# Performance work log

Measured on AMD Instinct MI355X. Metric: run time of the kernel, lower is better.

## Reference

```python
import jax, jax.numpy as jnp
from jax import lax
import numpy as np

N, M, S = 16, 32, 128
ALPHA = 1e-06


def _conv(x, w, b, stride):
    y = lax.conv_general_dilated(x, w, (stride, stride), [(1, 1), (1, 1)],
                                 dimension_numbers=('NCHW', 'OIHW', 'NCHW'))
    return y + b[None, :, None, None]


def _deconv(x, w, b):
    # torch ConvTranspose2d(k=4, s=2, p=1); torch weight layout [in, out, kh, kw]
    k = jnp.transpose(w, (1, 0, 2, 3))[:, :, ::-1, ::-1]
    y = lax.conv_general_dilated(x, k, (1, 1), [(2, 2), (2, 2)],
                                 lhs_dilation=(2, 2),
                                 dimension_numbers=('NCHW', 'OIHW', 'NCHW'))
    return y + b[None, :, None, None]


def _kaiming(key, shape):
    fan_in = shape[1] * shape[2] * shape[3]
    return jax.random.normal(key, shape, dtype=jnp.float32) * np.float32(np.sqrt(2.0 / fan_in))


def setup_inputs():
    key = jax.random.key(0)
    ks = jax.random.split(key, 12)
    B, H, W = 8, 256, 256
    return {
        'x': jax.random.normal(ks[0], (B, 3, H, W), dtype=jnp.float32),
        'e0n_w1': _kaiming(ks[1], (N, 3, 3, 3)), 'e0n_b1': jnp.zeros((N,), jnp.float32),
        'e0n_w2': _kaiming(ks[2], (N, N, 3, 3)), 'e0n_b2': jnp.zeros((N,), jnp.float32),
        'e0s_w1': _kaiming(ks[3], (S, 3, 3, 3)), 'e0s_b1': jnp.zeros((S,), jnp.float32),
        'e0s_w2': _kaiming(ks[4], (S, S, 3, 3)), 'e0s_b2': jnp.zeros((S,), jnp.float32),
        'd0_dw': jax.random.normal(ks[5], (S, 3, 4, 4), jnp.float32) * np.float32(np.sqrt(2.0 / (3 * 16))),
        'd0_db': jnp.zeros((3,), jnp.float32),
        'd0_cw': _kaiming(ks[6], (3, 3, 3, 3)), 'd0_cb': jnp.zeros((3,), jnp.float32),
        'cell_k': jax.random.normal(ks[7], (M, N), jnp.float32) / np.float32(np.sqrt(N)),
        'cell_v': jax.random.normal(ks[8], (M, S), jnp.float32) / np.float32(np.sqrt(S)),
    }


def reference(x, e0n_w1, e0n_b1, e0n_w2, e0n_b2, e0s_w1, e0s_b1, e0s_w2, e0s_b2,
              d0_dw, d0_db, d0_cw, d0_cb, cell_k, cell_v):
    silu = jax.nn.silu
    # ConvBlock encoders (stride-2 on second conv)
    e0_n = silu(_conv(silu(_conv(x, e0n_w1, e0n_b1, 1)), e0n_w2, e0n_b2, 2))  # [B,N,H/2,W/2]
    e0_s = silu(_conv(silu(_conv(x, e0s_w1, e0s_b1, 1)), e0s_w2, e0s_b2, 2))  # [B,S,H/2,W/2]
    B, _, H, W = e0_n.shape
    # permute+flatten to token streams (the irregular-access glue)
    z = e0_n.transpose(0, 2, 3, 1).reshape(-1, N)        # [T, N]
    t_star = e0_s.transpose(0, 2, 3, 1).reshape(-1, S)   # [T, S]
    # memcell: softmax key/value retrieval over M slots
    w = jax.nn.softmax(z @ cell_k.T / jnp.sqrt(jnp.float32(N)), axis=-1)  # [T, M]
    t_hat = w @ cell_v                                   # read_update's read (old memory)
    cell_v_new = cell_v + ALPHA * (w.T @ (t_star - t_hat))  # delta-rule value update
    t_read = w @ cell_v_new                              # read(); d1_n == e0_n so weights reused
    d0_m = t_read.reshape(B, H, W, S).transpose(0, 3, 1, 2)  # [B,S,H/2,W/2]
    # DeconvBlock decoder back to 3 channels at full resolution
    d0_n = silu(_conv(silu(_deconv(d0_m, d0_dw, d0_db)), d0_cw, d0_cb, 1))
    return d0_n
```

## Files before the change

### kernel.cpp

```cpp
#include <hip/hip_runtime.h>
#include <hip/hip_bf16.h>


#define ALPHA_F 1e-6f
#define TTOT 131072

typedef __attribute__((ext_vector_type(8))) short bf16x8;
typedef __attribute__((ext_vector_type(4))) float f32x4;

__device__ __forceinline__ float silu_f(float x) {
    return x * __builtin_amdgcn_rcpf(1.f + __expf(-x));
}

__device__ __forceinline__ short f2bf(float f) {
    __hip_bfloat16 h = __float2bfloat16(f);
    union { __hip_bfloat16 b; short s; } u; u.b = h; return u.s;
}

__device__ __forceinline__ float bf2f(unsigned short s) {
    union { unsigned u; float f; } c; c.u = (unsigned)s << 16; return c.f;
}

__device__ __forceinline__ int pack_fp8x4(float a, float b, float c, float d) {
    int lo = __builtin_amdgcn_cvt_pk_fp8_f32(a, b, 0, false);
    return  __builtin_amdgcn_cvt_pk_fp8_f32(c, d, lo, true);
}

template<int CO>
__global__ __launch_bounds__(256) void conv1_silu(
    const float* __restrict__ x, const float* __restrict__ wgt,
    const float* __restrict__ bias, float* __restrict__ out)
{
    int idx = blockIdx.x * 256 + threadIdx.x;
    int w = idx & 255, h = (idx >> 8) & 255, b = idx >> 16;
    const float* xb = x + (size_t)b * 3 * 65536;
    float in[27];
#pragma unroll
    for (int ci = 0; ci < 3; ci++)
#pragma unroll
        for (int ky = 0; ky < 3; ky++)
#pragma unroll
            for (int kx = 0; kx < 3; kx++) {
                int hh = h + ky - 1, ww = w + kx - 1;
                bool ok = ((unsigned)hh < 256u) && ((unsigned)ww < 256u);
                in[(ci * 3 + ky) * 3 + kx] = ok ? xb[(ci << 16) + (hh << 8) + ww] : 0.f;
            }
    float* ob = out + (size_t)b * CO * 65536 + (h << 8) + w;
#pragma unroll 4
    for (int co = 0; co < CO; co++) {
        float acc = bias[co];
#pragma unroll
        for (int k = 0; k < 27; k++) acc += in[k] * wgt[co * 27 + k];
        ob[(size_t)co << 16] = silu_f(acc);
    }
}

#define XPAD_DW 842112
__global__ __launch_bounds__(256) void sprep_kern(
    const float* __restrict__ x, const float* __restrict__ w1,
    unsigned* __restrict__ xpad, unsigned* __restrict__ wbf)
{
    if (blockIdx.x == 3290) {
        int co = threadIdx.x;
        if (co < 128) {
            unsigned short row[28];
#pragma unroll
            for (int k = 0; k < 27; k++) row[k] = (unsigned short)f2bf(w1[co * 27 + k]);
            row[27] = 0;
#pragma unroll
            for (int j = 0; j < 14; j++)
                wbf[co * 20 + j] = (unsigned)row[2 * j] | ((unsigned)row[2 * j + 1] << 16);
#pragma unroll
            for (int j = 14; j < 20; j++) wbf[co * 20 + j] = 0u;
        }
        return;
    }
    int d = blockIdx.x * 256 + threadIdx.x;
    if (d >= XPAD_DW) return;
    int w2 = d % 136;
    int rr = d / 136;
    int hp = rr % 258;
    int plane = rr / 258;
    unsigned val = 0u;
    if (hp >= 1 && hp <= 256 && w2 >= 4 && w2 <= 131) {
        const float* src = x + (size_t)plane * 65536 + (size_t)(hp - 1) * 256 + (2 * w2 - 8);
        float2 f = *(const float2*)src;
        val = (unsigned)(unsigned short)f2bf(f.x) |
              ((unsigned)(unsigned short)f2bf(f.y) << 16);
    }
    xpad[d] = val;
}

#define C1K 40
__global__ __launch_bounds__(256) void conv1s_mfma(
    const unsigned short* __restrict__ xpad, const unsigned short* __restrict__ wbf,
    const float* __restrict__ bias, char* __restrict__ out8)
{
    __shared__ __align__(16) short Ps[128 * C1K];
    int tid = threadIdx.x;
    int g = blockIdx.x;
    int b = g >> 10, rem = g & 1023;
    int hh2 = rem >> 1;
    int h = hh2 >> 1, w0 = (hh2 & 1) * 128;
    int coB = (rem & 1) * 64;

    int lane = tid & 63, wave = tid >> 6;
    int coL = (wave & 1) * 32, pxH = (wave >> 1) * 64;
    int r16 = lane & 15, q = lane >> 4, koff = q * 8;

    bf16x8 af[2];
#pragma unroll
    for (int mt = 0; mt < 2; mt++)
        af[mt] = *(const bf16x8*)&wbf[(coB + coL + mt * 16 + r16) * C1K + koff];

    if (tid < 128) {
        int wpix = w0 + tid;
        const unsigned short* p0 = xpad + ((size_t)(b * 3) * 258 + h) * 272 + 7 + wpix;
        unsigned v[27];
#pragma unroll
        for (int ci = 0; ci < 3; ci++) {
            const unsigned short* pc = p0 + ci * 70176;
#pragma unroll
            for (int ky = 0; ky < 3; ky++)
#pragma unroll
                for (int kx = 0; kx < 3; kx++)
                    v[ci * 9 + ky * 3 + kx] = pc[ky * 272 + kx];
        }
        unsigned dw[16];
#pragma unroll
        for (int i = 0; i < 13; i++) dw[i] = v[2 * i] | (v[2 * i + 1] << 16);
        dw[13] = v[26];
        dw[14] = 0u; dw[15] = 0u;
#pragma unroll
        for (int j = 0; j < 4; j++)
            *(float4*)&Ps[tid * C1K + j * 8] = *(float4*)&dw[j * 4];
    }
    __syncthreads();

    bf16x8 bfr[4];
#pragma unroll
    for (int nt = 0; nt < 4; nt++)
        bfr[nt] = *(bf16x8*)&Ps[(pxH + nt * 16 + r16) * C1K + koff];
    f32x4 acc[2][4];
#pragma unroll
    for (int mt = 0; mt < 2; mt++)
#pragma unroll
        for (int nt = 0; nt < 4; nt++) {
#pragma unroll
            for (int r = 0; r < 4; r++) acc[mt][nt][r] = 0.f;
            acc[mt][nt] = __builtin_amdgcn_mfma_f32_16x16x32_bf16(
                af[mt], bfr[nt], acc[mt][nt], 0, 0, 0);
        }

    int hwb = (h << 8) + w0 + pxH;
    int* ob4 = (int*)out8 + (size_t)b * 8 * 65536 * 4;
#pragma unroll
    for (int mt = 0; mt < 2; mt++) {
        int cb = coB + coL + mt * 16 + q * 4;
        float4 bv = *(const float4*)&bias[cb];
        int cg = (coB + coL + mt * 16) >> 4;
#pragma unroll
        for (int nt = 0; nt < 4; nt++) {
            int hw = hwb + nt * 16 + r16;
            int pk = pack_fp8x4(silu_f(acc[mt][nt][0] + bv.x),
                                silu_f(acc[mt][nt][1] + bv.y),
                                silu_f(acc[mt][nt][2] + bv.z),
                                silu_f(acc[mt][nt][3] + bv.w));
            ob4[((size_t)cg * 65536 + hw) * 4 + q] = pk;
        }
    }
}

__global__ __launch_bounds__(256) void wprep_kern(
    const float* __restrict__ w, int* __restrict__ wt8)
{
    int d = blockIdx.x * 256 + threadIdx.x;
    int pos = d >> 12;
    int rb = (d << 2) & 16383;
    int c16 = rb >> 11, co = (rb >> 4) & 127, e0 = rb & 15;
    float f[4];
#pragma unroll
    for (int j = 0; j < 4; j++) {
        int ci = c16 * 16 + e0 + j;
        f[j] = w[co * 1152 + ci * 9 + pos];
    }
    wt8[d] = pack_fp8x4(f[0], f[1], f[2], f[3]);
}

__global__ __launch_bounds__(256) void conv2s_mfma(
    const char* __restrict__ a8,
    const char* __restrict__ wt8,
    const float* __restrict__ bias, __hip_bfloat16* __restrict__ out)
{
    __shared__ __align__(16) char As[4 * 64 * 16];
    __shared__ __align__(16) char Bs[4 * 128 * 16];
    int tid = threadIdx.x;
    int g = blockIdx.x;
    int b = g >> 8, h2 = (g >> 1) & 127, w2base = (g & 1) * 64;
    int lane = tid & 63, wave = tid >> 6;
    int mrow = lane & 15, q = lane >> 4;

    f32x4 acc[2][4];
#pragma unroll
    for (int i = 0; i < 2; i++)
#pragma unroll
        for (int j = 0; j < 4; j++)
#pragma unroll
            for (int r = 0; r < 4; r++) acc[i][j][r] = 0.f;

    const float4* ab4 = (const float4*)a8 + (size_t)b * 8 * 65536;
    const float4* wb4 = (const float4*)wt8;
    int cA = tid >> 6, tokA = tid & 63;
    int sB0 = tid, sB1 = tid + 256;

#pragma unroll 1
    for (int pos = 0; pos < 9; pos++) {
        int ky = pos / 3, kx = pos - 3 * ky;
        int y = 2 * h2 - 1 + ky;
        if ((unsigned)y >= 256u) continue;
        int x = 2 * (w2base + tokA) - 1 + kx;
        int pix = (y << 8) + (x & 255);
#pragma unroll 1
        for (int cc = 0; cc < 2; cc++) {
            float4 a0 = make_float4(0.f, 0.f, 0.f, 0.f);
            if (x >= 0) a0 = ab4[(size_t)(cc * 4 + cA) * 65536 + pix];
            const float4* brow = wb4 + pos * 1024 + cc * 512;
            float4 b0 = brow[sB0], b1 = brow[sB1];
            __syncthreads();
            *(float4*)&As[tid * 16] = a0;
            *(float4*)&Bs[sB0 * 16] = b0;
            *(float4*)&Bs[sB1 * 16] = b1;
            __syncthreads();
#pragma unroll
            for (int kc = 0; kc < 2; kc++) {
                int cl = kc * 2 + (q >> 1), off = (q & 1) * 8;
                long afr[4], bfr[2];
#pragma unroll
                for (int mt = 0; mt < 4; mt++)
                    afr[mt] = *(long*)&As[(cl * 64 + mt * 16 + mrow) * 16 + off];
#pragma unroll
                for (int nt = 0; nt < 2; nt++)
                    bfr[nt] = *(long*)&Bs[(cl * 128 + wave * 32 + nt * 16 + mrow) * 16 + off];
#pragma unroll
                for (int nt = 0; nt < 2; nt++)
#pragma unroll
                    for (int mt = 0; mt < 4; mt++)
                        acc[nt][mt] = __builtin_amdgcn_mfma_f32_16x16x32_fp8_fp8(
                            afr[mt], bfr[nt], acc[nt][mt], 0, 0, 0);
            }
        }
    }
    int rowg = q * 4;
    size_t tbase = (size_t)g * 64;
#pragma unroll
    for (int nt = 0; nt < 2; nt++) {
        int co = wave * 32 + nt * 16 + mrow;
        float bvs = bias[co];
#pragma unroll
        for (int mt = 0; mt < 4; mt++)
#pragma unroll
            for (int r = 0; r < 4; r++) {
                int m = mt * 16 + rowg + r;
                out[(tbase + m) * 128 + co] =
                    __float2bfloat16(silu_f(acc[nt][mt][r] + bvs));
            }
    }
}

__global__ __launch_bounds__(256) void conv2n_fused(
    const float* __restrict__ in, const float* __restrict__ wgt,
    const float* __restrict__ bias, const float* __restrict__ ck,
    float* __restrict__ wout)
{
    int idx = blockIdx.x * 256 + threadIdx.x;
    int w2 = idx & 127, h2 = (idx >> 7) & 127, b = idx >> 14;
    const float* ib = in + (size_t)b * 16 * 65536;
    float acc[16];
#pragma unroll
    for (int co = 0; co < 16; co++) acc[co] = bias[co];
    int h0 = 2 * h2 - 1, w0 = 2 * w2 - 1;
    for (int ci = 0; ci < 16; ci++) {
        float t[9];
#pragma unroll
        for (int ky = 0; ky < 3; ky++)
#pragma unroll
            for (int kx = 0; kx < 3; kx++) {
                int hh = h0 + ky, ww = w0 + kx;
                bool ok = ((unsigned)hh < 256u) && ((unsigned)ww < 256u);
                t[ky * 3 + kx] = ok ? ib[((size_t)ci << 16) + (hh << 8) + ww] : 0.f;
            }
#pragma unroll
        for (int co = 0; co < 16; co++)
#pragma unroll
            for (int k = 0; k < 9; k++)
                acc[co] += t[k] * wgt[(co * 16 + ci) * 9 + k];
    }
    float zv[16];
#pragma unroll
    for (int co = 0; co < 16; co++) zv[co] = silu_f(acc[co]);
    float lg[32]; float mx = -1e30f;
#pragma unroll
    for (int m = 0; m < 32; m++) {
        float a = 0.f;
#pragma unroll
        for (int n = 0; n < 16; n++) a += zv[n] * ck[m * 16 + n];
        a *= 0.25f;
        lg[m] = a; mx = fmaxf(mx, a);
    }
    float s = 0.f;
#pragma unroll
    for (int m = 0; m < 32; m++) { lg[m] = __expf(lg[m] - mx); s += lg[m]; }
    float inv = 1.f / s;
    float4* wp = (float4*)(wout + (size_t)idx * 32);
#pragma unroll
    for (int m = 0; m < 8; m++)
        wp[m] = make_float4(lg[4 * m] * inv, lg[4 * m + 1] * inv,
                            lg[4 * m + 2] * inv, lg[4 * m + 3] * inv);
}

__global__ __launch_bounds__(256) void memcell_acc_kern(
    const float* __restrict__ wmat, const __hip_bfloat16* __restrict__ tstar,
    float* __restrict__ part)
{
    __shared__ float ws[64][32];
    __shared__ float ts[64 * 128];
    int tid = threadIdx.x;
    int sg = tid & 31, mg = tid >> 5;
    int mW = tid & 31, m2 = (tid >> 5) * 4;
    float accT[16], accW[4];
#pragma unroll
    for (int i = 0; i < 16; i++) accT[i] = 0.f;
#pragma unroll
    for (int i = 0; i < 4; i++) accW[i] = 0.f;

#pragma unroll 1
    for (int cc = 0; cc < 2; cc++) {
        int c = blockIdx.x * 2 + cc;
        size_t base = (size_t)c * 64;
        __syncthreads();
        {
            const float4* src = (const float4*)(wmat + base * 32);
            float4* dst = (float4*)&ws[0][0];
#pragma unroll
            for (int i = 0; i < 2; i++) dst[tid + 256 * i] = src[tid + 256 * i];
            const float4* src2 = (const float4*)(tstar + base * 128);
#pragma unroll
            for (int i = 0; i < 4; i++) {
                union { float4 v; unsigned short us[8]; } u;
                u.v = src2[tid + 256 * i];
                float* d = &ts[(tid + 256 * i) * 8];
                float4 lo = make_float4(bf2f(u.us[0]), bf2f(u.us[1]), bf2f(u.us[2]), bf2f(u.us[3]));
                float4 hi = make_float4(bf2f(u.us[4]), bf2f(u.us[5]), bf2f(u.us[6]), bf2f(u.us[7]));
                *(float4*)d = lo; *(float4*)(d + 4) = hi;
            }
        }
        __syncthreads();
        for (int t = 0; t < 64; t++) {
            float4 wv = *(const float4*)&ws[t][mg * 4];
            float4 sv = *(const float4*)&ts[t * 128 + sg * 4];
            accT[0]  += wv.x * sv.x; accT[1]  += wv.x * sv.y; accT[2]  += wv.x * sv.z; accT[3]  += wv.x * sv.w;
            accT[4]  += wv.y * sv.x; accT[5]  += wv.y * sv.y; accT[6]  += wv.y * sv.z; accT[7]  += wv.y * sv.w;
            accT[8]  += wv.z * sv.x; accT[9]  += wv.z * sv.y; accT[10] += wv.z * sv.z; accT[11] += wv.z * sv.w;
            accT[12] += wv.w * sv.x; accT[13] += wv.w * sv.y; accT[14] += wv.w * sv.z; accT[15] += wv.w * sv.w;
            float wa = ws[t][mW];
            float4 wb = *(const float4*)&ws[t][m2];
            accW[0] += wa * wb.x; accW[1] += wa * wb.y;
            accW[2] += wa * wb.z; accW[3] += wa * wb.w;
        }
    }
    float* pb = part + (size_t)blockIdx.x * 5120;
#pragma unroll
    for (int i = 0; i < 16; i++) pb[i * 256 + tid] = accT[i];
#pragma unroll
    for (int i = 0; i < 4; i++) pb[4096 + i * 256 + tid] = accW[i];
}

__global__ __launch_bounds__(256) void memcell_reduce_kern(
    const float* __restrict__ part, float* __restrict__ WtT, float* __restrict__ WtW)
{
    int gid = blockIdx.x * 256 + threadIdx.x;
    int j = gid % 5120, seg = gid / 5120;
    const float* p = part + (size_t)seg * 64 * 5120 + j;
    float s = 0.f;
#pragma unroll 8
    for (int k = 0; k < 64; k++) s += p[(size_t)k * 5120];
    int i = j >> 8, t = j & 255;
    if (j < 4096) {
        int sg = t & 31, mg = t >> 5;
        atomicAdd(&WtT[(mg * 4 + (i >> 2)) * 128 + sg * 4 + (i & 3)], s);
    } else {
        int i2 = i - 16;
        int mW = t & 31, m2 = (t >> 5) * 4;
        atomicAdd(&WtW[mW * 32 + m2 + i2], s);
    }
}

__global__ __launch_bounds__(256) void cvnew_kern(
    const float* __restrict__ cv, const float* __restrict__ WtW,
    const float* __restrict__ WtT, float* __restrict__ cvn)
{
    int idx = blockIdx.x * 256 + threadIdx.x;
    int s = idx & 127, m = idx >> 7;
    float g = WtT[idx];
#pragma unroll
    for (int j = 0; j < 32; j++) g -= WtW[m * 32 + j] * cv[j * 128 + s];
    cvn[idx] = cv[idx] + ALPHA_F * g;
}

__global__ __launch_bounds__(256) void emat_kern(
    const float* __restrict__ cvn, const float* __restrict__ dw, float* __restrict__ E)
{
    int idx = blockIdx.x * 256 + threadIdx.x;
    int m = idx >> 6, j = idx & 63;
    int pos = j >> 2, co = j & 3;
    float s = 0.f;
    if (co < 3) {
        const float* cv = cvn + m * 128;
        for (int ci = 0; ci < 128; ci++)
            s += cv[ci] * dw[ci * 48 + co * 16 + pos];
    }
    E[idx] = s;
}

__global__ __launch_bounds__(256) void tread64_kern(
    const float* __restrict__ wmat, const float* __restrict__ E, float* __restrict__ t64)
{
    int t = blockIdx.x * 256 + threadIdx.x;
    float wv[32];
    const float4* wp = (const float4*)(wmat + (size_t)t * 32);
#pragma unroll
    for (int i = 0; i < 8; i++) {
        float4 v = wp[i];
        wv[4 * i] = v.x; wv[4 * i + 1] = v.y; wv[4 * i + 2] = v.z; wv[4 * i + 3] = v.w;
    }
    f32x4 acc[16];
#pragma unroll
    for (int i = 0; i < 16; i++)
#pragma unroll
        for (int r = 0; r < 4; r++) acc[i][r] = 0.f;
    const f32x4* E4 = (const f32x4*)E;
#pragma unroll 4
    for (int m = 0; m < 32; m++) {
        float wm = wv[m];
#pragma unroll
        for (int i = 0; i < 16; i++) {
            f32x4 e = E4[m * 16 + i];
#pragma unroll
            for (int r = 0; r < 4; r++) acc[i][r] += wm * e[r];
        }
    }
    f32x4* ob = (f32x4*)t64;
#pragma unroll
    for (int i = 0; i < 16; i++)
        ob[(size_t)i * TTOT + t] = acc[i];
}

__global__ __launch_bounds__(256) void dec_gather_kern(
    const float* __restrict__ t64, const float* __restrict__ db, float* __restrict__ out)
{
    int g = blockIdx.x;
    int wb = g & 7, hb = (g >> 3) & 7, b = g >> 6;
    int tx = threadIdx.x & 15, ty = threadIdx.x >> 4;
    int h2 = hb * 16 + ty, w2 = wb * 16 + tx;

    float mh[3], mw[3];
    int ihc[3], iwc[3];
#pragma unroll
    for (int a = 0; a < 3; a++) {
        int v = h2 - 1 + a;
        mh[a] = ((unsigned)v < 128u) ? 1.f : 0.f;
        ihc[a] = v < 0 ? 0 : (v > 127 ? 127 : v);
        v = w2 - 1 + a;
        mw[a] = ((unsigned)v < 128u) ? 1.f : 0.f;
        iwc[a] = v < 0 ? 0 : (v > 127 ? 127 : v);
    }
    float acc[2][2][3];
#pragma unroll
    for (int ph = 0; ph < 2; ph++)
#pragma unroll
        for (int pw = 0; pw < 2; pw++)
#pragma unroll
            for (int co = 0; co < 3; co++) acc[ph][pw][co] = db[co];

    const int RA[4] = {0, 1, 1, 2}, RP[4] = {0, 0, 1, 1}, RK[4] = {3, 1, 2, 0};
    size_t tokb = (size_t)b * 16384;
#pragma unroll
    for (int ri = 0; ri < 4; ri++)
#pragma unroll
        for (int cj = 0; cj < 4; cj++) {
            int a = RA[ri], c = RA[cj];
            float m = mh[a] * mw[c];
            size_t tok = tokb + (ihc[a] << 7) + iwc[c];
            int pos = RK[ri] * 4 + RK[cj];
            float4 v = *(const float4*)&t64[((size_t)pos * TTOT + tok) * 4];
            int ph = RP[ri], pw = RP[cj];
            acc[ph][pw][0] += m * v.x;
            acc[ph][pw][1] += m * v.y;
            acc[ph][pw][2] += m * v.z;
        }
    int h = 2 * h2, w = 2 * w2;
#pragma unroll
    for (int ph = 0; ph < 2; ph++)
#pragma unroll
        for (int co = 0; co < 3; co++) {
            float2 v = make_float2(silu_f(acc[ph][0][co]), silu_f(acc[ph][1][co]));
            *(float2*)&out[(size_t)b * 3 * 65536 + (size_t)co * 65536 + ((size_t)(h + ph) << 8) + w] = v;
        }
}

extern "C" void kernel_launch(void* const* d_in, const int* in_sizes, int n_in,
                              void* d_out, int out_size, void* d_ws, size_t ws_size,
                              hipStream_t stream)
{
    const float* x      = (const float*)d_in[0];
    const float* e0n_w1 = (const float*)d_in[1];
    const float* e0n_b1 = (const float*)d_in[2];
    const float* e0n_w2 = (const float*)d_in[3];
    const float* e0n_b2 = (const float*)d_in[4];
    const float* e0s_w1 = (const float*)d_in[5];
    const float* e0s_b1 = (const float*)d_in[6];
    const float* e0s_w2 = (const float*)d_in[7];
    const float* e0s_b2 = (const float*)d_in[8];
    const float* d0_dw  = (const float*)d_in[9];
    const float* d0_db  = (const float*)d_in[10];
    const float* d0_cw  = (const float*)d_in[11];
    const float* d0_cb  = (const float*)d_in[12];
    const float* cell_k = (const float*)d_in[13];
    const float* cell_v = (const float*)d_in[14];
    float* outp = (float*)d_out;

    char* ws = (char*)d_ws;
    char* a_s8             = ws;
    __hip_bfloat16* t_star = (__hip_bfloat16*)(ws + 134217728);
    float* a_n    = (float*)(ws + 201326592);
    char* wt8     = (char*)(ws + 201326592);
    float* part   = (float*)(ws + 201850880);
    float* Emat   = (float*)(ws + 224000000);
    float* wmat   = (float*)(ws + 243269632);
    float* WtW    = (float*)(ws + 260046848);
    float* WtT    = (float*)(ws + 260050944);
    float* cvn    = (float*)(ws + 260067328);
    float* t64    = (float*)(ws);
    float* dec1   = (float*)(ws + 67108864);
    unsigned* xpad = (unsigned*)(ws + 73400320);
    unsigned* wbf  = (unsigned*)(ws + 76800000);

    sprep_kern<<<3291, 256, 0, stream>>>(x, e0s_w1, xpad, wbf);
    conv1_silu<16><<<2048, 256, 0, stream>>>(x, e0n_w1, e0n_b1, a_n);
    conv2n_fused<<<512, 256, 0, stream>>>(a_n, e0n_w2, e0n_b2, cell_k, wmat);
    wprep_kern<<<144, 256, 0, stream>>>(e0s_w2, (int*)wt8);
    conv1s_mfma<<<8192, 256, 0, stream>>>((const unsigned short*)xpad,
                                          (const unsigned short*)wbf, e0s_b1, a_s8);
    conv2s_mfma<<<2048, 256, 0, stream>>>(a_s8, wt8, e0s_b2, t_star);
    hipMemsetAsync(WtW, 0, (1024 + 4096) * sizeof(float), stream);
    memcell_acc_kern<<<1024, 256, 0, stream>>>(wmat, t_star, part);
    memcell_reduce_kern<<<320, 256, 0, stream>>>(part, WtT, WtW);
    cvnew_kern<<<16, 256, 0, stream>>>(cell_v, WtW, WtT, cvn);
    emat_kern<<<8, 256, 0, stream>>>(cvn, d0_dw, Emat);
    tread64_kern<<<512, 256, 0, stream>>>(wmat, Emat, t64);
    dec_gather_kern<<<512, 256, 0, stream>>>(t64, d0_db, dec1);
    conv1_silu<3><<<2048, 256, 0, stream>>>(dec1, d0_cw, d0_cb, outp);
}
```

Before: 282.8 us.

## Double-buffer LDS in stride-2 FP8 conv with swizzled layout and top-row skip

Converts the conv2s_mfma main loop into a double-buffered software pipeline: global loads for the next (pos, channel-chunk) stage are issued before computing the current stage, and there is one barrier per stage instead of two. It also XOR-swizzles the 8-byte halves in LDS to reduce bank conflicts, and starts the position loop at 3 when h2==0 instead of testing each position. LDS usage doubles and register pressure rises from holding prefetched data. The last-row case (y=256) is never reached for stride 2, so dropping the bounds check is safe.

```diff
diff --git a/kernel.cpp b/kernel.cpp
--- a/kernel.cpp
+++ b/kernel.cpp
@@ -192,8 +192,8 @@
     const char* __restrict__ wt8,
     const float* __restrict__ bias, __hip_bfloat16* __restrict__ out)
 {
-    __shared__ __align__(16) char As[4 * 64 * 16];
-    __shared__ __align__(16) char Bs[4 * 128 * 16];
+    __shared__ __align__(16) char As[2][4096];
+    __shared__ __align__(16) char Bs[2][8192];
     int tid = threadIdx.x;
     int g = blockIdx.x;
     int b = g >> 8, h2 = (g >> 1) & 127, w2base = (g & 1) * 64;
@@ -212,44 +212,77 @@
     const float4* wb4 = (const float4*)wt8;
     int cA = tid >> 6, tokA = tid & 63;
     int sB0 = tid, sB1 = tid + 256;
-
-#pragma unroll 1
-    for (int pos = 0; pos < 9; pos++) {
-        int ky = pos / 3, kx = pos - 3 * ky;
-        int y = 2 * h2 - 1 + ky;
-        if ((unsigned)y >= 256u) continue;
-        int x = 2 * (w2base + tokA) - 1 + kx;
-        int pix = (y << 8) + (x & 255);
-#pragma unroll 1
-        for (int cc = 0; cc < 2; cc++) {
-            float4 a0 = make_float4(0.f, 0.f, 0.f, 0.f);
-            if (x >= 0) a0 = ab4[(size_t)(cc * 4 + cA) * 65536 + pix];
-            const float4* brow = wb4 + pos * 1024 + cc * 512;
-            float4 b0 = brow[sB0], b1 = brow[sB1];
-            __syncthreads();
-            *(float4*)&As[tid * 16] = a0;
-            *(float4*)&Bs[sB0 * 16] = b0;
-            *(float4*)&Bs[sB1 * 16] = b1;
-            __syncthreads();
-#pragma unroll
-            for (int kc = 0; kc < 2; kc++) {
-                int cl = kc * 2 + (q >> 1), off = (q & 1) * 8;
-                long afr[4], bfr[2];
+    int swT = tid & 8;
+    int offA = ((q & 1) * 8) ^ (mrow & 8);
+
+    int ps = (h2 == 0) ? 3 : 0;
+    int nst = (9 - ps) * 2;
+
+#define C2S_LOAD(s, ra, rb0, rb1) do {                                      \
+        int pos_ = ps + ((s) >> 1), cc_ = (s) & 1;                          \
+        int ky_ = pos_ / 3, kx_ = pos_ - 3 * ky_;                           \
+        int y_ = 2 * h2 - 1 + ky_;                                          \
+        int x_ = 2 * (w2base + tokA) - 1 + kx_;                             \
+        int pix_ = (y_ << 8) + (x_ & 255);                                  \
+        ra = make_float4(0.f, 0.f, 0.f, 0.f);                               \
+        if (x_ >= 0) ra = ab4[(size_t)(cc_ * 4 + cA) * 65536 + pix_];       \
+        const float4* brow_ = wb4 + pos_ * 1024 + cc_ * 512;                \
+        rb0 = brow_[sB0]; rb1 = brow_[sB1];                                 \
+    } while (0)
+
+#define C2S_STORE(bufi, ra, rb0, rb1) do {                                  \
+        union { float4 v; long l[2]; } uA_, u0_, u1_;                       \
+        uA_.v = ra; u0_.v = rb0; u1_.v = rb1;                               \
+        *(long*)&As[bufi][tid * 16 + swT]       = uA_.l[0];                 \
+        *(long*)&As[bufi][tid * 16 + (8 ^ swT)] = uA_.l[1];                 \
+        *(long*)&Bs[bufi][sB0 * 16 + swT]       = u0_.l[0];                 \
+        *(long*)&Bs[bufi][sB0 * 16 + (8 ^ swT)] = u0_.l[1];                 \
+        *(long*)&Bs[bufi][sB1 * 16 + swT]       = u1_.l[0];                 \
+        *(long*)&Bs[bufi][sB1 * 16 + (8 ^ swT)] = u1_.l[1];                 \
+    } while (0)
+
+    auto compute = [&](const char* Ab, const char* Bb) {
+#pragma unroll
+        for (int kc = 0; kc < 2; kc++) {
+            int cl = kc * 2 + (q >> 1);
+            long afr[4], bfr[2];
+#pragma unroll
+            for (int mt = 0; mt < 4; mt++)
+                afr[mt] = *(const long*)&Ab[(cl * 64 + mt * 16 + mrow) * 16 + offA];
+#pragma unroll
+            for (int nt = 0; nt < 2; nt++)
+                bfr[nt] = *(const long*)&Bb[(cl * 128 + wave * 32 + nt * 16 + mrow) * 16 + offA];
+#pragma unroll
+            for (int nt = 0; nt < 2; nt++)
 #pragma unroll
                 for (int mt = 0; mt < 4; mt++)
-                    afr[mt] = *(long*)&As[(cl * 64 + mt * 16 + mrow) * 16 + off];
-#pragma unroll
-                for (int nt = 0; nt < 2; nt++)
-                    bfr[nt] = *(long*)&Bs[(cl * 128 + wave * 32 + nt * 16 + mrow) * 16 + off];
-#pragma unroll
-                for (int nt = 0; nt < 2; nt++)
-#pragma unroll
-                    for (int mt = 0; mt < 4; mt++)
-                        acc[nt][mt] = __builtin_amdgcn_mfma_f32_16x16x32_fp8_fp8(
-                            afr[mt], bfr[nt], acc[nt][mt], 0, 0, 0);
-            }
-        }
-    }
+                    acc[nt][mt] = __builtin_amdgcn_mfma_f32_16x16x32_fp8_fp8(
+                        afr[mt], bfr[nt], acc[nt][mt], 0, 0, 0);
+        }
+    };
+
+    {
+        float4 ra, rb0, rb1;
+        C2S_LOAD(0, ra, rb0, rb1);
+        C2S_STORE(0, ra, rb0, rb1);
+    }
+    __syncthreads();
+
+    for (int s = 0; s < nst; s += 2) {
+        float4 na, nb0, nb1;
+        C2S_LOAD(s + 1, na, nb0, nb1);
+        compute(As[0], Bs[0]);
+        C2S_STORE(1, na, nb0, nb1);
+        __syncthreads();
+        bool more = (s + 2 < nst);
+        if (more) C2S_LOAD(s + 2, na, nb0, nb1);
+        compute(As[1], Bs[1]);
+        if (more) C2S_STORE(0, na, nb0, nb1);
+        __syncthreads();
+    }
+#undef C2S_LOAD
+#undef C2S_STORE
+
     int rowg = q * 4;
     size_t tbase = (size_t)g * 64;
 #pragma unroll
```

Result: no change. 281.8 us (-0.3%).

## Double-buffer conv2s A tiles and load B fragments directly from global

Applied to the files above, without the earlier changes.

Restructures the stride-2 128-channel conv MFMA loop into a two-stage software pipeline. The next kernel position's activation tile is prefetched into registers while MFMAs run on the current LDS buffer, with one barrier per position instead of two per channel chunk. Weight fragments are now read straight from global into registers rather than staged through LDS, and the A tile uses an XOR swizzle to cut LDS bank conflicts. Both channel chunks are merged into one step per position. The cost is higher register pressure and more global weight traffic per wave. Also relies on the B-weight layout from the prep kernel matching the new global indexing.

```diff
diff --git a/kernel.cpp b/kernel.cpp
--- a/kernel.cpp
+++ b/kernel.cpp
@@ -192,8 +192,7 @@
     const char* __restrict__ wt8,
     const float* __restrict__ bias, __hip_bfloat16* __restrict__ out)
 {
-    __shared__ __align__(16) char As[4 * 64 * 16];
-    __shared__ __align__(16) char Bs[4 * 128 * 16];
+    __shared__ __align__(16) char As[2][8192];
     int tid = threadIdx.x;
     int g = blockIdx.x;
     int b = g >> 8, h2 = (g >> 1) & 127, w2base = (g & 1) * 64;
@@ -209,47 +208,94 @@
             for (int r = 0; r < 4; r++) acc[i][j][r] = 0.f;
 
     const float4* ab4 = (const float4*)a8 + (size_t)b * 8 * 65536;
-    const float4* wb4 = (const float4*)wt8;
     int cA = tid >> 6, tokA = tid & 63;
-    int sB0 = tid, sB1 = tid + 256;
-
-#pragma unroll 1
-    for (int pos = 0; pos < 9; pos++) {
-        int ky = pos / 3, kx = pos - 3 * ky;
-        int y = 2 * h2 - 1 + ky;
-        if ((unsigned)y >= 256u) continue;
-        int x = 2 * (w2base + tokA) - 1 + kx;
-        int pix = (y << 8) + (x & 255);
-#pragma unroll 1
-        for (int cc = 0; cc < 2; cc++) {
-            float4 a0 = make_float4(0.f, 0.f, 0.f, 0.f);
-            if (x >= 0) a0 = ab4[(size_t)(cc * 4 + cA) * 65536 + pix];
-            const float4* brow = wb4 + pos * 1024 + cc * 512;
-            float4 b0 = brow[sB0], b1 = brow[sB1];
-            __syncthreads();
-            *(float4*)&As[tid * 16] = a0;
-            *(float4*)&Bs[sB0 * 16] = b0;
-            *(float4*)&Bs[sB1 * 16] = b1;
-            __syncthreads();
-#pragma unroll
-            for (int kc = 0; kc < 2; kc++) {
-                int cl = kc * 2 + (q >> 1), off = (q & 1) * 8;
-                long afr[4], bfr[2];
+    int swT = tid & 8;
+    int offA = ((q & 1) * 8) ^ (mrow & 8);
+    const char* wb = wt8;
+    int bbase = (q >> 1) * 2048 + (wave * 32 + mrow) * 16 + (q & 1) * 8;
+
+    int ps = (h2 == 0) ? 3 : 0;
+
+#define C2S_LOADA(pos_, ra0, ra1) do {                                      \
+        int ky_ = (pos_) / 3, kx_ = (pos_) - 3 * ky_;                       \
+        int y_ = 2 * h2 - 1 + ky_;                                          \
+        int x_ = 2 * (w2base + tokA) - 1 + kx_;                             \
+        int pix_ = (y_ << 8) + (x_ & 255);                                  \
+        ra0 = make_float4(0.f, 0.f, 0.f, 0.f); ra1 = ra0;                   \
+        if (x_ >= 0) {                                                      \
+            ra0 = ab4[(size_t)cA * 65536 + pix_];                           \
+            ra1 = ab4[(size_t)(cA + 4) * 65536 + pix_];                     \
+        }                                                                   \
+    } while (0)
+
+#define C2S_LOADB(pos_, dst) do {                                           \
+        const char* bp_ = wb + (pos_) * 16384 + bbase;                      \
+        _Pragma("unroll")                                                   \
+        for (int kc_ = 0; kc_ < 4; kc_++)                                   \
+            _Pragma("unroll")                                               \
+            for (int nt_ = 0; nt_ < 2; nt_++)                               \
+                dst[kc_ * 2 + nt_] = *(const long*)(bp_ + kc_ * 4096 + nt_ * 256); \
+    } while (0)
+
+#define C2S_STOREA(bufi, ra0, ra1) do {                                     \
+        union { float4 v; long l[2]; } u0_, u1_;                            \
+        u0_.v = ra0; u1_.v = ra1;                                           \
+        *(long*)&As[bufi][tid * 16 + swT]               = u0_.l[0];         \
+        *(long*)&As[bufi][tid * 16 + (8 ^ swT)]         = u0_.l[1];         \
+        *(long*)&As[bufi][(tid + 256) * 16 + swT]       = u1_.l[0];         \
+        *(long*)&As[bufi][(tid + 256) * 16 + (8 ^ swT)] = u1_.l[1];         \
+    } while (0)
+
+    auto compute = [&](const char* Ab, const long (&bf)[8]) {
+#pragma unroll
+        for (int kc = 0; kc < 4; kc++) {
+            int cl = kc * 2 + (q >> 1);
+            long afr[4];
+#pragma unroll
+            for (int mt = 0; mt < 4; mt++)
+                afr[mt] = *(const long*)&Ab[(cl * 64 + mt * 16 + mrow) * 16 + offA];
+#pragma unroll
+            for (int nt = 0; nt < 2; nt++)
 #pragma unroll
                 for (int mt = 0; mt < 4; mt++)
-                    afr[mt] = *(long*)&As[(cl * 64 + mt * 16 + mrow) * 16 + off];
-#pragma unroll
-                for (int nt = 0; nt < 2; nt++)
-                    bfr[nt] = *(long*)&Bs[(cl * 128 + wave * 32 + nt * 16 + mrow) * 16 + off];
-#pragma unroll
-                for (int nt = 0; nt < 2; nt++)
-#pragma unroll
-                    for (int mt = 0; mt < 4; mt++)
-                        acc[nt][mt] = __builtin_amdgcn_mfma_f32_16x16x32_fp8_fp8(
-                            afr[mt], bfr[nt], acc[nt][mt], 0, 0, 0);
-            }
-        }
-    }
+                    acc[nt][mt] = __builtin_amdgcn_mfma_f32_16x16x32_fp8_fp8(
+                        afr[mt], bf[kc * 2 + nt], acc[nt][mt], 0, 0, 0);
+        }
+    };
+
+    long bA[8], bB[8];
+    float4 pa0, pa1;
+    C2S_LOADA(ps, pa0, pa1);
+    C2S_LOADB(ps, bA);
+    C2S_STOREA(0, pa0, pa1);
+    __syncthreads();
+
+    int pos = ps;
+    int nleft = 9 - ps;
+    while (true) {
+        if (nleft > 1) {
+            C2S_LOADA(pos + 1, pa0, pa1);
+            C2S_LOADB(pos + 1, bB);
+        }
+        compute(As[0], bA);
+        if (nleft > 1) C2S_STOREA(1, pa0, pa1);
+        __syncthreads();
+        if (nleft == 1) break;
+        pos++; nleft--;
+        if (nleft > 1) {
+            C2S_LOADA(pos + 1, pa0, pa1);
+            C2S_LOADB(pos + 1, bA);
+        }
+        compute(As[1], bB);
+        if (nleft > 1) C2S_STOREA(0, pa0, pa1);
+        __syncthreads();
+        if (nleft == 1) break;
+        pos++; nleft--;
+    }
+#undef C2S_LOADA
+#undef C2S_LOADB
+#undef C2S_STOREA
+
     int rowg = q * 4;
     size_t tbase = (size_t)g * 64;
 #pragma unroll
```

After: 277.3 us. No clear change (-1.9%).
